# Optimization experiments

Measured on AMD Instinct MI355X. Metric: run time of the kernel, lower is better.

Reference implementation:

```python
import jax, jax.numpy as jnp
import numpy as np

E = 1024        # embedding_dim
H = 16          # num_heads
DR = 1          # downsample_rate
INT = E // DR   # internal_dim
HD = INT // H   # head dim
B, NQ, NK = 4, 2048, 2048


def setup_inputs() -> dict:
    key = jax.random.key(0)
    ks = jax.random.split(key, 11)
    s_in = 1.0 / np.sqrt(E)
    s_int = 1.0 / np.sqrt(INT)
    return {
        "q": jax.random.normal(ks[0], (B, NQ, E), jnp.float32),
        "k": jax.random.normal(ks[1], (B, NK, E), jnp.float32),
        "v": jax.random.normal(ks[2], (B, NK, E), jnp.float32),
        "wq": jax.random.normal(ks[3], (E, INT), jnp.float32) * s_in,
        "bq": jnp.zeros((INT,), jnp.float32),
        "wk": jax.random.normal(ks[4], (E, INT), jnp.float32) * s_in,
        "bk": jnp.zeros((INT,), jnp.float32),
        "wv": jax.random.normal(ks[5], (E, INT), jnp.float32) * s_in,
        "bv": jnp.zeros((INT,), jnp.float32),
        "wo": jax.random.normal(ks[6], (INT, E), jnp.float32) * s_int,
        "bo": jnp.zeros((E,), jnp.float32),
    }


def _heads(x):
    # (B, N, INT) -> (B, H, N, HD)
    b, n, c = x.shape
    return x.reshape(b, n, H, c // H).transpose(0, 2, 1, 3)


def reference(q, k, v, wq, bq, wk, bk, wv, bv, wo, bo):
    qh = _heads(q @ wq + bq)          # (B,H,NQ,HD)
    kh = _heads(k @ wk + bk)          # (B,H,NK,HD)
    vh = _heads(v @ wv + bv)          # (B,H,NK,HD)
    scale = 1.0 / np.sqrt(HD)
    attn = jnp.einsum('bhqd,bhkd->bhqk', qh, kh) * scale  # (B,H,NQ,NK)
    attn = jax.nn.softmax(attn, axis=-1)
    out = jnp.einsum('bhqk,bhkd->bhqd', attn, vh)          # (B,H,NQ,HD)
    out = out.transpose(0, 2, 1, 3).reshape(q.shape[0], qh.shape[2], INT)
    return out @ wo + bo
```

## Files before the change

kernel.cpp:

```cpp
#include <hip/hip_runtime.h>
#include <hip/hip_bf16.h>
#include <cstdint>
#include <cstddef>

typedef __bf16 bf16_t;
typedef __bf16 bf16x8 __attribute__((ext_vector_type(8)));
typedef float f32x4 __attribute__((ext_vector_type(4)));
typedef float f32x16 __attribute__((ext_vector_type(16)));
typedef uint32_t u32;

#define EDIM 1024
#define HH 16
#define HD 64
#define NSEQ 2048
#define QSCALE 0.18033688011f

__device__ __forceinline__ void async_copy16(const bf16_t* gsrc, bf16_t* lds_dst) {
    __builtin_amdgcn_global_load_lds(
        (const __attribute__((address_space(1))) uint32_t*)gsrc,
        (__attribute__((address_space(3))) uint32_t*)lds_dst,
        16, 0, 0);
}

__device__ __forceinline__ bf16x8 cvt8(float4 x, float4 y) {
    bf16x8 v = {(bf16_t)x.x, (bf16_t)x.y, (bf16_t)x.z, (bf16_t)x.w,
                (bf16_t)y.x, (bf16_t)y.y, (bf16_t)y.z, (bf16_t)y.w};
    return v;
}

__global__ void cvt3_f32_bf16(const float* __restrict__ q, const float* __restrict__ k,
                              const float* __restrict__ v,
                              bf16_t* __restrict__ xq, bf16_t* __restrict__ xk,
                              bf16_t* __restrict__ xv) {
    const float* in;
    bf16_t* out;
    switch (blockIdx.y) {
        case 0: in = q; out = xq; break;
        case 1: in = k; out = xk; break;
        default: in = v; out = xv; break;
    }
    size_t i = ((size_t)blockIdx.x * 256 + threadIdx.x) * 8;
    float4 x = *(const float4*)(in + i);
    float4 y = *(const float4*)(in + i + 4);
    *(bf16x8*)(out + i) = cvt8(x, y);
}

__global__ void transpose_all(const float* __restrict__ w0, const float* __restrict__ w1,
                              const float* __restrict__ w2, const float* __restrict__ w3,
                              bf16_t* __restrict__ o0, bf16_t* __restrict__ o1,
                              bf16_t* __restrict__ o2, bf16_t* __restrict__ o3) {
    __shared__ bf16_t t[64][65];
    const float* in;
    bf16_t* out;
    switch (blockIdx.z) {
        case 0: in = w0; out = o0; break;
        case 1: in = w1; out = o1; break;
        case 2: in = w2; out = o2; break;
        default: in = w3; out = o3; break;
    }
    const int tid = threadIdx.x;
    const int kt = blockIdx.x, nt = blockIdx.y;
    #pragma unroll
    for (int i = 0; i < 16; i++) {
        int idx = i * 256 + tid;
        int r = idx >> 6, c = idx & 63;
        t[r][c] = (bf16_t)in[(size_t)(kt * 64 + r) * 1024 + nt * 64 + c];
    }
    __syncthreads();
    #pragma unroll
    for (int i = 0; i < 16; i++) {
        int idx = i * 256 + tid;
        int r = idx >> 6, c = idx & 63;
        out[(size_t)(nt * 64 + r) * 1024 + kt * 64 + c] = t[c][r];
    }
}

__global__ __launch_bounds__(256, 2)
void gemm_qkv_async(const bf16_t* __restrict__ Xq, const bf16_t* __restrict__ Xk,
                    const bf16_t* __restrict__ Xv,
                    const bf16_t* __restrict__ Wq, const bf16_t* __restrict__ Wk,
                    const bf16_t* __restrict__ Wv,
                    const float* __restrict__ bq, const float* __restrict__ bk,
                    const float* __restrict__ bv,
                    bf16_t* __restrict__ Qh, bf16_t* __restrict__ Kh,
                    bf16_t* __restrict__ Vt) {
    constexpr int BM = 128, BN = 128, BK = 64, K = 1024, NT = K / BK;
    __shared__ bf16_t Asm[2][BM * BK];
    __shared__ bf16_t Bsm[2][BN * BK];
    const int tid = threadIdx.x;
    const int wave = tid >> 6, lane = tid & 63;
    const int quad = lane >> 4, l15 = lane & 15;
    const int bx = blockIdx.x, by = blockIdx.y;
    const int mt = (by >> 3) * 8 + bx;
    const int n0 = (by & 7) * BN;
    const int wt = mt >> 6;
    const int m0 = (mt - wt * 64) * BM;
    const int wm = (wave & 1) * 64, wn = (wave >> 1) * 64;

    const bf16_t* A    = wt == 0 ? Xq : (wt == 1 ? Xk : Xv);
    const bf16_t* Bt   = wt == 0 ? Wq : (wt == 1 ? Wk : Wv);
    const float*  bias = wt == 0 ? bq : (wt == 1 ? bk : bv);
    bf16_t*       Cout = wt == 0 ? Qh : (wt == 1 ? Kh : Vt);
    const float oscale = wt == 0 ? QSCALE : 1.0f;

    f32x4 acc[4][4] = {};

    auto stage = [&](int t, int buf) {
        const int k0 = t * BK;
        #pragma unroll
        for (int i = 0; i < 4; i++) {
            int s = i * 256 + tid;
            int row = s >> 3, kc = (s & 7) ^ (row & 7);
            async_copy16(A + (size_t)(m0 + row) * K + k0 + kc * 8, &Asm[buf][s * 8]);
        }
        #pragma unroll
        for (int i = 0; i < 4; i++) {
            int s = i * 256 + tid;
            int row = s >> 3, kc = (s & 7) ^ (row & 7);
            async_copy16(Bt + (size_t)(n0 + row) * K + k0 + kc * 8, &Bsm[buf][s * 8]);
        }
    };

    stage(0, 0);
    stage(1, 1);
    asm volatile("s_waitcnt vmcnt(8)" ::: "memory");
    __builtin_amdgcn_s_barrier();
    __builtin_amdgcn_sched_barrier(0);

    for (int t = 0; t < NT; ++t) {
        const int buf = t & 1;
        bf16x8 af[2][4], bfr[2][4];
        #pragma unroll
        for (int ks = 0; ks < 2; ks++) {
            #pragma unroll
            for (int mi = 0; mi < 4; mi++) {
                int row = wm + mi * 16 + l15;
                int g = ks * 4 + quad;
                af[ks][mi] = *(const bf16x8*)&Asm[buf][row * BK + ((g ^ (row & 7)) * 8)];
            }
            #pragma unroll
            for (int ni = 0; ni < 4; ni++) {
                int row = wn + ni * 16 + l15;
                int g = ks * 4 + quad;
                bfr[ks][ni] = *(const bf16x8*)&Bsm[buf][row * BK + ((g ^ (row & 7)) * 8)];
            }
        }
        #pragma unroll
        for (int ks = 0; ks < 2; ks++)
            #pragma unroll
            for (int mi = 0; mi < 4; mi++)
                #pragma unroll
                for (int ni = 0; ni < 4; ni++)
                    acc[mi][ni] = __builtin_amdgcn_mfma_f32_16x16x32_bf16(
                        af[ks][mi], bfr[ks][ni], acc[mi][ni], 0, 0, 0);

        if (t + 1 < NT) {
            __builtin_amdgcn_s_barrier();
            __builtin_amdgcn_sched_barrier(0);
            if (t + 2 < NT) {
                stage(t + 2, buf);
                asm volatile("s_waitcnt vmcnt(8)" ::: "memory");
            } else {
                asm volatile("s_waitcnt vmcnt(0)" ::: "memory");
            }
            asm volatile("s_waitcnt lgkmcnt(0)" ::: "memory");
            __builtin_amdgcn_s_barrier();
            __builtin_amdgcn_sched_barrier(0);
        }
    }

    #pragma unroll
    for (int mi = 0; mi < 4; mi++) {
        #pragma unroll
        for (int ni = 0; ni < 4; ni++) {
            #pragma unroll
            for (int r = 0; r < 4; r++) {
                int m = m0 + wm + mi * 16 + quad * 4 + r;
                int nch = n0 + wn + ni * 16 + l15;
                float v = (acc[mi][ni][r] + bias[nch]) * oscale;
                int b = m >> 11, n = m & 2047;
                int h = nch >> 6, d = nch & 63;
                if (wt < 2)
                    Cout[(((size_t)(b * HH + h)) * NSEQ + n) * HD + d] = (bf16_t)v;
                else
                    Cout[(((size_t)(b * HH + h)) * HD + d) * NSEQ + n] = (bf16_t)v;
            }
        }
    }
}

__global__ __launch_bounds__(256, 2)
void gemm_qkv(const float* __restrict__ Aq, const float* __restrict__ Ak,
              const float* __restrict__ Av,
              const bf16_t* __restrict__ Wq, const bf16_t* __restrict__ Wk,
              const bf16_t* __restrict__ Wv,
              const float* __restrict__ bq, const float* __restrict__ bk,
              const float* __restrict__ bv,
              bf16_t* __restrict__ Qh, bf16_t* __restrict__ Kh,
              bf16_t* __restrict__ Vt) {
    constexpr int BM = 128, BN = 128, BK = 64, K = 1024, NT = K / BK;
    __shared__ bf16_t Asm[2][BM * BK];
    __shared__ bf16_t Bsm[2][BN * BK];
    const int tid = threadIdx.x;
    const int wave = tid >> 6, lane = tid & 63;
    const int quad = lane >> 4, l15 = lane & 15;
    const int bx = blockIdx.x, by = blockIdx.y;
    const int mt = (by >> 3) * 8 + bx;
    const int n0 = (by & 7) * BN;
    const int wt = mt >> 6;
    const int m0 = (mt - wt * 64) * BM;
    const int wm = (wave & 1) * 64, wn = (wave >> 1) * 64;

    const float*  A    = wt == 0 ? Aq : (wt == 1 ? Ak : Av);
    const bf16_t* Bt   = wt == 0 ? Wq : (wt == 1 ? Wk : Wv);
    const float*  bias = wt == 0 ? bq : (wt == 1 ? bk : bv);
    bf16_t*       Cout = wt == 0 ? Qh : (wt == 1 ? Kh : Vt);
    const float oscale = wt == 0 ? QSCALE : 1.0f;

    f32x4 acc[4][4] = {};
    float4 ar[8];

    auto loadA = [&](int t) {
        const int k0 = t * BK;
        #pragma unroll
        for (int i = 0; i < 4; i++) {
            int s = i * 256 + tid;
            int row = s >> 3, kc = (s & 7) ^ (row & 7);
            const float* sp = A + (size_t)(m0 + row) * K + k0 + kc * 8;
            ar[2 * i]     = *(const float4*)sp;
            ar[2 * i + 1] = *(const float4*)(sp + 4);
        }
    };
    auto writeA = [&](int buf) {
        #pragma unroll
        for (int i = 0; i < 4; i++) {
            int s = i * 256 + tid;
            *(bf16x8*)&Asm[buf][s * 8] = cvt8(ar[2 * i], ar[2 * i + 1]);
        }
    };
    auto stageB = [&](int t, int buf) {
        const int k0 = t * BK;
        #pragma unroll
        for (int i = 0; i < 4; i++) {
            int s = i * 256 + tid;
            int row = s >> 3, kc = (s & 7) ^ (row & 7);
            async_copy16(Bt + (size_t)(n0 + row) * K + k0 + kc * 8, &Bsm[buf][s * 8]);
        }
    };

    loadA(0);
    stageB(0, 0);
    writeA(0);
    stageB(1, 1);
    asm volatile("s_waitcnt vmcnt(4)" ::: "memory");
    loadA(1);
    asm volatile("s_waitcnt lgkmcnt(0)" ::: "memory");
    __builtin_amdgcn_s_barrier();
    __builtin_amdgcn_sched_barrier(0);

    for (int t = 0; t < NT; ++t) {
        const int buf = t & 1;
        bf16x8 af[2][4], bfr[2][4];
        #pragma unroll
        for (int ks = 0; ks < 2; ks++) {
            #pragma unroll
            for (int mi = 0; mi < 4; mi++) {
                int row = wm + mi * 16 + l15;
                int g = ks * 4 + quad;
                af[ks][mi] = *(const bf16x8*)&Asm[buf][row * BK + ((g ^ (row & 7)) * 8)];
            }
            #pragma unroll
            for (int ni = 0; ni < 4; ni++) {
                int row = wn + ni * 16 + l15;
                int g = ks * 4 + quad;
                bfr[ks][ni] = *(const bf16x8*)&Bsm[buf][row * BK + ((g ^ (row & 7)) * 8)];
            }
        }
        #pragma unroll
        for (int ks = 0; ks < 2; ks++)
            #pragma unroll
            for (int mi = 0; mi < 4; mi++)
                #pragma unroll
                for (int ni = 0; ni < 4; ni++)
                    acc[mi][ni] = __builtin_amdgcn_mfma_f32_16x16x32_bf16(
                        af[ks][mi], bfr[ks][ni], acc[mi][ni], 0, 0, 0);

        if (t + 1 < NT) {
            __builtin_amdgcn_s_barrier();
            __builtin_amdgcn_sched_barrier(0);
            writeA(buf ^ 1);
            if (t + 2 < NT) {
                stageB(t + 2, buf);
                asm volatile("s_waitcnt vmcnt(4)" ::: "memory");
                loadA(t + 2);
            } else {
                asm volatile("s_waitcnt vmcnt(0)" ::: "memory");
            }
            asm volatile("s_waitcnt lgkmcnt(0)" ::: "memory");
            __builtin_amdgcn_s_barrier();
            __builtin_amdgcn_sched_barrier(0);
        }
    }

    #pragma unroll
    for (int mi = 0; mi < 4; mi++) {
        #pragma unroll
        for (int ni = 0; ni < 4; ni++) {
            #pragma unroll
            for (int r = 0; r < 4; r++) {
                int m = m0 + wm + mi * 16 + quad * 4 + r;
                int nch = n0 + wn + ni * 16 + l15;
                float v = (acc[mi][ni][r] + bias[nch]) * oscale;
                int b = m >> 11, n = m & 2047;
                int h = nch >> 6, d = nch & 63;
                if (wt < 2)
                    Cout[(((size_t)(b * HH + h)) * NSEQ + n) * HD + d] = (bf16_t)v;
                else
                    Cout[(((size_t)(b * HH + h)) * HD + d) * NSEQ + n] = (bf16_t)v;
            }
        }
    }
}

__global__ __launch_bounds__(256, 2)
void gemm_out(const bf16_t* __restrict__ A, const bf16_t* __restrict__ Bt,
              const float* __restrict__ bias, float* __restrict__ C) {
    constexpr int BM = 128, BN = 128, BK = 64, K = 1024, N = 1024, NT = K / BK;
    __shared__ bf16_t Asm[2][BM * BK];
    __shared__ bf16_t Bsm[2][BN * BK];
    const int tid = threadIdx.x;
    const int wave = tid >> 6, lane = tid & 63;
    const int quad = lane >> 4, l15 = lane & 15;
    const int bx = blockIdx.x, by = blockIdx.y;
    const int n0 = (by & 7) * BN;
    const int m0 = ((by >> 3) * 8 + bx) * BM;
    const int wm = (wave & 1) * 64, wn = (wave >> 1) * 64;

    f32x4 acc[4][4] = {};

    auto stage = [&](int t, int buf) {
        const int k0 = t * BK;
        #pragma unroll
        for (int i = 0; i < 4; i++) {
            int s = i * 256 + tid;
            int row = s >> 3, kc = (s & 7) ^ (row & 7);
            async_copy16(A + (size_t)(m0 + row) * K + k0 + kc * 8, &Asm[buf][s * 8]);
        }
        #pragma unroll
        for (int i = 0; i < 4; i++) {
            int s = i * 256 + tid;
            int row = s >> 3, kc = (s & 7) ^ (row & 7);
            async_copy16(Bt + (size_t)(n0 + row) * K + k0 + kc * 8, &Bsm[buf][s * 8]);
        }
    };

    stage(0, 0);
    stage(1, 1);
    asm volatile("s_waitcnt vmcnt(8)" ::: "memory");
    __builtin_amdgcn_s_barrier();
    __builtin_amdgcn_sched_barrier(0);

    for (int t = 0; t < NT; ++t) {
        const int buf = t & 1;
        bf16x8 af[2][4], bfr[2][4];
        #pragma unroll
        for (int ks = 0; ks < 2; ks++) {
            #pragma unroll
            for (int mi = 0; mi < 4; mi++) {
                int row = wm + mi * 16 + l15;
                int g = ks * 4 + quad;
                af[ks][mi] = *(const bf16x8*)&Asm[buf][row * BK + ((g ^ (row & 7)) * 8)];
            }
            #pragma unroll
            for (int ni = 0; ni < 4; ni++) {
                int row = wn + ni * 16 + l15;
                int g = ks * 4 + quad;
                bfr[ks][ni] = *(const bf16x8*)&Bsm[buf][row * BK + ((g ^ (row & 7)) * 8)];
            }
        }
        #pragma unroll
        for (int ks = 0; ks < 2; ks++)
            #pragma unroll
            for (int mi = 0; mi < 4; mi++)
                #pragma unroll
                for (int ni = 0; ni < 4; ni++)
                    acc[mi][ni] = __builtin_amdgcn_mfma_f32_16x16x32_bf16(
                        af[ks][mi], bfr[ks][ni], acc[mi][ni], 0, 0, 0);

        if (t + 1 < NT) {
            __builtin_amdgcn_s_barrier();
            __builtin_amdgcn_sched_barrier(0);
            if (t + 2 < NT) {
                stage(t + 2, buf);
                asm volatile("s_waitcnt vmcnt(8)" ::: "memory");
            } else {
                asm volatile("s_waitcnt vmcnt(0)" ::: "memory");
            }
            asm volatile("s_waitcnt lgkmcnt(0)" ::: "memory");
            __builtin_amdgcn_s_barrier();
            __builtin_amdgcn_sched_barrier(0);
        }
    }

    #pragma unroll
    for (int mi = 0; mi < 4; mi++) {
        #pragma unroll
        for (int ni = 0; ni < 4; ni++) {
            #pragma unroll
            for (int r = 0; r < 4; r++) {
                int m = m0 + wm + mi * 16 + quad * 4 + r;
                int nch = n0 + wn + ni * 16 + l15;
                C[(size_t)m * N + nch] = acc[mi][ni][r] + bias[nch];
            }
        }
    }
}

union PW { u32 w[4]; bf16x8 v; };

__device__ __forceinline__ u32 pack_bf16(float lo, float hi) {
    union { bf16_t h[2]; u32 u; } x;
    x.h[0] = (bf16_t)lo;
    x.h[1] = (bf16_t)hi;
    return x.u;
}

__device__ __forceinline__ void half_swap(u32& a, u32& b) {
    auto r = __builtin_amdgcn_permlane32_swap(a, b, false, false);
    a = r[0];
    b = r[1];
}

__device__ __forceinline__ void softmax_pack(const f32x16 sa, float* lp,
                                             PW& f0, PW& f1) {
    float p[16];
    #pragma unroll
    for (int r = 0; r < 16; r++) {
        p[r] = __builtin_amdgcn_exp2f(sa[r]);
        lp[r & 3] += p[r];
    }
    u32 x0 = pack_bf16(p[0],  p[1]),  x1 = pack_bf16(p[2],  p[3]);
    u32 x2 = pack_bf16(p[4],  p[5]),  x3 = pack_bf16(p[6],  p[7]);
    u32 x4 = pack_bf16(p[8],  p[9]),  x5 = pack_bf16(p[10], p[11]);
    u32 x6 = pack_bf16(p[12], p[13]), x7 = pack_bf16(p[14], p[15]);
    half_swap(x0, x2); half_swap(x1, x3);
    half_swap(x4, x6); half_swap(x5, x7);
    f0.w[0] = x0; f0.w[1] = x1; f0.w[2] = x2; f0.w[3] = x3;
    f1.w[0] = x4; f1.w[1] = x5; f1.w[2] = x6; f1.w[3] = x7;
}

__global__ __launch_bounds__(256, 4)
void attn_kernel(const bf16_t* __restrict__ Qh, const bf16_t* __restrict__ Kh,
                 const bf16_t* __restrict__ Vt, bf16_t* __restrict__ out) {
    __shared__ bf16_t Ks[2][64 * 64];
    __shared__ bf16_t Vs[2][64 * 64];
    const int tid = threadIdx.x, wave = tid >> 6, lane = tid & 63;
    const int l31 = lane & 31, hi = lane >> 5;
    const int B = blockIdx.x;
    const int qt = (B >> 3) & 15;
    const int bh = (B >> 7) * 8 + (B & 7);
    const int b = bh >> 4, h = bh & 15;

    const bf16_t* kbase = Kh + (size_t)bh * NSEQ * HD;
    const bf16_t* vbase = Vt + (size_t)bh * HD * NSEQ;

    bf16x8 qf[4];
    {
        const bf16_t* qrow =
            Qh + ((size_t)bh * NSEQ + qt * 128 + wave * 32 + l31) * HD + hi * 8;
        #pragma unroll
        for (int s = 0; s < 4; s++) qf[s] = *(const bf16x8*)(qrow + s * 16);
    }

    const bf16_t *ks0, *ks1, *vs0, *vs1;
    {
        int r0 = tid >> 3, c0 = tid & 7;
        int s1 = tid + 256;
        int r1 = s1 >> 3, c1 = s1 & 7;
        ks0 = kbase + r0 * HD + (c0 ^ (r0 & 7)) * 8;
        ks1 = kbase + r1 * HD + (c1 ^ (r1 & 7)) * 8;
        vs0 = vbase + (size_t)r0 * NSEQ + (c0 ^ (r0 & 7)) * 8;
        vs1 = vbase + (size_t)r1 * NSEQ + (c1 ^ (r1 & 7)) * 8;
    }

    async_copy16(ks0, &Ks[0][tid * 8]);
    async_copy16(ks1, &Ks[0][(tid + 256) * 8]);
    async_copy16(vs0, &Vs[0][tid * 8]);
    async_copy16(vs1, &Vs[0][(tid + 256) * 8]);

    f32x16 oacc[2] = {};
    float lp[4] = {};

    for (int t = 0; t < 32; t++) {
        const int cur = t & 1;
        __syncthreads();

        if (t < 31) {
            ks0 += 64 * HD; ks1 += 64 * HD;
            vs0 += 64;      vs1 += 64;
            async_copy16(ks0, &Ks[cur ^ 1][tid * 8]);
            async_copy16(ks1, &Ks[cur ^ 1][(tid + 256) * 8]);
            async_copy16(vs0, &Vs[cur ^ 1][tid * 8]);
            async_copy16(vs1, &Vs[cur ^ 1][(tid + 256) * 8]);
        }

        const f32x16 zero = {};
        f32x16 sacc0, sacc1;
        {
            int g = hi;
            int row0 = l31, row1 = 32 + l31;
            bf16x8 ak0 = *(const bf16x8*)&Ks[cur][row0 * 64 + ((g ^ (row0 & 7)) * 8)];
            bf16x8 ak1 = *(const bf16x8*)&Ks[cur][row1 * 64 + ((g ^ (row1 & 7)) * 8)];
            __builtin_amdgcn_s_setprio(1);
            sacc0 = __builtin_amdgcn_mfma_f32_32x32x16_bf16(ak0, qf[0], zero, 0, 0, 0);
            sacc1 = __builtin_amdgcn_mfma_f32_32x32x16_bf16(ak1, qf[0], zero, 0, 0, 0);
            __builtin_amdgcn_s_setprio(0);
        }
        #pragma unroll
        for (int s = 1; s < 4; s++) {
            int g = s * 2 + hi;
            int row0 = l31;
            int row1 = 32 + l31;
            bf16x8 ak0 = *(const bf16x8*)&Ks[cur][row0 * 64 + ((g ^ (row0 & 7)) * 8)];
            bf16x8 ak1 = *(const bf16x8*)&Ks[cur][row1 * 64 + ((g ^ (row1 & 7)) * 8)];
            __builtin_amdgcn_s_setprio(1);
            sacc0 = __builtin_amdgcn_mfma_f32_32x32x16_bf16(ak0, qf[s], sacc0, 0, 0, 0);
            sacc1 = __builtin_amdgcn_mfma_f32_32x32x16_bf16(ak1, qf[s], sacc1, 0, 0, 0);
            __builtin_amdgcn_s_setprio(0);
        }

        PW pa[4];
        softmax_pack(sacc0, lp, pa[0], pa[1]);
        softmax_pack(sacc1, lp, pa[2], pa[3]);

        #pragma unroll
        for (int dt = 0; dt < 2; dt++) {
            #pragma unroll
            for (int ks = 0; ks < 4; ks++) {
                int row = dt * 32 + l31;
                int g = ks * 2 + hi;
                bf16x8 bv = *(const bf16x8*)&Vs[cur][row * 64 + ((g ^ (row & 7)) * 8)];
                __builtin_amdgcn_s_setprio(1);
                oacc[dt] = __builtin_amdgcn_mfma_f32_32x32x16_bf16(
                    pa[ks].v, bv, oacc[dt], 0, 0, 0);
                __builtin_amdgcn_s_setprio(0);
            }
        }
    }

    float lsum = (lp[0] + lp[1]) + (lp[2] + lp[3]);
    lsum += __shfl_xor(lsum, 32, 64);
    float linv = 1.f / lsum;
    float rinv[16];
    #pragma unroll
    for (int r = 0; r < 16; r++) {
        int q = (r & 3) + 8 * (r >> 2) + 4 * hi;
        rinv[r] = __shfl(linv, q, 64);
    }

    const int n0 = qt * 128 + wave * 32;
    #pragma unroll
    for (int dt = 0; dt < 2; dt++) {
        int c = h * 64 + dt * 32 + l31;
        #pragma unroll
        for (int r = 0; r < 16; r++) {
            int q = (r & 3) + 8 * (r >> 2) + 4 * hi;
            out[((size_t)b * NSEQ + n0 + q) * EDIM + c] = (bf16_t)(oacc[dt][r] * rinv[r]);
        }
    }
}

extern "C" void kernel_launch(void* const* d_in, const int* in_sizes, int n_in,
                              void* d_out, int out_size, void* d_ws, size_t ws_size,
                              hipStream_t stream) {
    const float* q  = (const float*)d_in[0];
    const float* k  = (const float*)d_in[1];
    const float* v  = (const float*)d_in[2];
    const float* wq = (const float*)d_in[3];
    const float* bq = (const float*)d_in[4];
    const float* wk = (const float*)d_in[5];
    const float* bk = (const float*)d_in[6];
    const float* wv = (const float*)d_in[7];
    const float* bv = (const float*)d_in[8];
    const float* wo = (const float*)d_in[9];
    const float* bo = (const float*)d_in[10];
    float* out = (float*)d_out;

    char* ws = (char*)d_ws;
    bf16_t* wqt = (bf16_t*)(ws + ((size_t)0  << 20));
    bf16_t* wkt = (bf16_t*)(ws + ((size_t)2  << 20));
    bf16_t* wvt = (bf16_t*)(ws + ((size_t)4  << 20));
    bf16_t* wot = (bf16_t*)(ws + ((size_t)6  << 20));

    bf16_t* Qh  = (bf16_t*)(ws + ((size_t)8  << 20));
    bf16_t* Kh  = (bf16_t*)(ws + ((size_t)24 << 20));
    bf16_t* Vt  = (bf16_t*)(ws + ((size_t)40 << 20));
    bf16_t* ao  = (bf16_t*)(ws + ((size_t)56 << 20));
    bf16_t* Xq  = (bf16_t*)(ws + ((size_t)72 << 20));
    bf16_t* Xk  = (bf16_t*)(ws + ((size_t)88 << 20));
    bf16_t* Xv  = (bf16_t*)(ws + ((size_t)104 << 20));

    const bool big = ws_size >= ((size_t)120 << 20);

    transpose_all<<<dim3(16, 16, 4), dim3(256), 0, stream>>>(wq, wk, wv, wo,
                                                             wqt, wkt, wvt, wot);

    if (big) {
        cvt3_f32_bf16<<<dim3(4096, 3), dim3(256), 0, stream>>>(q, k, v, Xq, Xk, Xv);
        gemm_qkv_async<<<dim3(8, 192), dim3(256), 0, stream>>>(Xq, Xk, Xv,
                                                               wqt, wkt, wvt,
                                                               bq, bk, bv, Qh, Kh, Vt);
    } else {
        gemm_qkv<<<dim3(8, 192), dim3(256), 0, stream>>>(q, k, v, wqt, wkt, wvt,
                                                         bq, bk, bv, Qh, Kh, Vt);
    }

    attn_kernel<<<1024, dim3(256), 0, stream>>>(Qh, Kh, Vt, ao);

    gemm_out<<<dim3(8, 64), dim3(256), 0, stream>>>(ao, wot, bo, out);
}
```

Measured before the change: 334.4 us.

## Merge prep kernels and compute softmax row sums with an MFMA against ones

Merges the weight-transpose and activation-conversion kernels into a single launch, removing one kernel launch and its tail. In attention, the per-lane scalar accumulation of exp values is replaced by an extra MFMA of the probabilities against a ones vector. That gives row sums already laid out like the output accumulator, so the final cross-lane shuffles are dropped. Launch bounds for the attention kernel are relaxed from 4 to 2 waves per SIMD, giving it more registers for the extra accumulator at the possible cost of occupancy.

Result: slower. 344.6 us (+3.1%).

```diff
diff --git a/kernel.cpp b/kernel.cpp
--- a/kernel.cpp
+++ b/kernel.cpp
@@ -28,50 +28,56 @@
     return v;
 }
 
-__global__ void cvt3_f32_bf16(const float* __restrict__ q, const float* __restrict__ k,
-                              const float* __restrict__ v,
-                              bf16_t* __restrict__ xq, bf16_t* __restrict__ xk,
-                              bf16_t* __restrict__ xv) {
-    const float* in;
-    bf16_t* out;
-    switch (blockIdx.y) {
-        case 0: in = q; out = xq; break;
-        case 1: in = k; out = xk; break;
-        default: in = v; out = xv; break;
-    }
-    size_t i = ((size_t)blockIdx.x * 256 + threadIdx.x) * 8;
-    float4 x = *(const float4*)(in + i);
-    float4 y = *(const float4*)(in + i + 4);
-    *(bf16x8*)(out + i) = cvt8(x, y);
-}
-
-__global__ void transpose_all(const float* __restrict__ w0, const float* __restrict__ w1,
-                              const float* __restrict__ w2, const float* __restrict__ w3,
-                              bf16_t* __restrict__ o0, bf16_t* __restrict__ o1,
-                              bf16_t* __restrict__ o2, bf16_t* __restrict__ o3) {
+__global__ void prep(const float* __restrict__ w0, const float* __restrict__ w1,
+                     const float* __restrict__ w2, const float* __restrict__ w3,
+                     bf16_t* __restrict__ o0, bf16_t* __restrict__ o1,
+                     bf16_t* __restrict__ o2, bf16_t* __restrict__ o3,
+                     const float* __restrict__ q, const float* __restrict__ k,
+                     const float* __restrict__ v,
+                     bf16_t* __restrict__ xq, bf16_t* __restrict__ xk,
+                     bf16_t* __restrict__ xv, int do_cvt) {
     __shared__ bf16_t t[64][65];
-    const float* in;
-    bf16_t* out;
-    switch (blockIdx.z) {
-        case 0: in = w0; out = o0; break;
-        case 1: in = w1; out = o1; break;
-        case 2: in = w2; out = o2; break;
-        default: in = w3; out = o3; break;
-    }
+    const int id = blockIdx.x;
     const int tid = threadIdx.x;
-    const int kt = blockIdx.x, nt = blockIdx.y;
-    #pragma unroll
-    for (int i = 0; i < 16; i++) {
-        int idx = i * 256 + tid;
-        int r = idx >> 6, c = idx & 63;
-        t[r][c] = (bf16_t)in[(size_t)(kt * 64 + r) * 1024 + nt * 64 + c];
-    }
-    __syncthreads();
-    #pragma unroll
-    for (int i = 0; i < 16; i++) {
-        int idx = i * 256 + tid;
-        int r = idx >> 6, c = idx & 63;
-        out[(size_t)(nt * 64 + r) * 1024 + kt * 64 + c] = t[c][r];
+    if (id < 1024) {
+        const int z = id >> 8, rem = id & 255, kt = rem >> 4, nt = rem & 15;
+        const float* in;
+        bf16_t* out;
+        switch (z) {
+            case 0: in = w0; out = o0; break;
+            case 1: in = w1; out = o1; break;
+            case 2: in = w2; out = o2; break;
+            default: in = w3; out = o3; break;
+        }
+        #pragma unroll
+        for (int i = 0; i < 16; i++) {
+            int idx = i * 256 + tid;
+            int r = idx >> 6, c = idx & 63;
+            t[r][c] = (bf16_t)in[(size_t)(kt * 64 + r) * 1024 + nt * 64 + c];
+        }
+        __syncthreads();
+        #pragma unroll
+        for (int i = 0; i < 16; i++) {
+            int idx = i * 256 + tid;
+            int r = idx >> 6, c = idx & 63;
+            out[(size_t)(nt * 64 + r) * 1024 + kt * 64 + c] = t[c][r];
+        }
+    } else {
+        if (!do_cvt) return;
+        const int j = id - 1024;
+        const int which = j >> 12;
+        const int blk = j & 4095;
+        const float* in;
+        bf16_t* out;
+        switch (which) {
+            case 0: in = q; out = xq; break;
+            case 1: in = k; out = xk; break;
+            default: in = v; out = xv; break;
+        }
+        size_t i = ((size_t)blk * 256 + tid) * 8;
+        float4 x = *(const float4*)(in + i);
+        float4 y = *(const float4*)(in + i + 4);
+        *(bf16x8*)(out + i) = cvt8(x, y);
     }
 }
 
@@ -431,14 +437,11 @@
     b = r[1];
 }
 
-__device__ __forceinline__ void softmax_pack(const f32x16 sa, float* lp,
-                                             PW& f0, PW& f1) {
+__device__ __forceinline__ void softmax_pack(const f32x16 sa, PW& f0, PW& f1) {
     float p[16];
     #pragma unroll
-    for (int r = 0; r < 16; r++) {
+    for (int r = 0; r < 16; r++)
         p[r] = __builtin_amdgcn_exp2f(sa[r]);
-        lp[r & 3] += p[r];
-    }
     u32 x0 = pack_bf16(p[0],  p[1]),  x1 = pack_bf16(p[2],  p[3]);
     u32 x2 = pack_bf16(p[4],  p[5]),  x3 = pack_bf16(p[6],  p[7]);
     u32 x4 = pack_bf16(p[8],  p[9]),  x5 = pack_bf16(p[10], p[11]);
@@ -449,7 +452,7 @@
     f1.w[0] = x4; f1.w[1] = x5; f1.w[2] = x6; f1.w[3] = x7;
 }
 
-__global__ __launch_bounds__(256, 4)
+__global__ __launch_bounds__(256, 2)
 void attn_kernel(const bf16_t* __restrict__ Qh, const bf16_t* __restrict__ Kh,
                  const bf16_t* __restrict__ Vt, bf16_t* __restrict__ out) {
     __shared__ bf16_t Ks[2][64 * 64];
@@ -488,8 +491,12 @@
     async_copy16(vs0, &Vs[0][tid * 8]);
     async_copy16(vs1, &Vs[0][(tid + 256) * 8]);
 
+    bf16x8 onesv;
+    #pragma unroll
+    for (int j = 0; j < 8; j++) onesv[j] = (bf16_t)1.0f;
+
     f32x16 oacc[2] = {};
-    float lp[4] = {};
+    f32x16 oacc_l = {};
 
     for (int t = 0; t < 32; t++) {
         const int cur = t & 1;
@@ -530,8 +537,15 @@
         }
 
         PW pa[4];
-        softmax_pack(sacc0, lp, pa[0], pa[1]);
-        softmax_pack(sacc1, lp, pa[2], pa[3]);
+        softmax_pack(sacc0, pa[0], pa[1]);
+        softmax_pack(sacc1, pa[2], pa[3]);
+
+        __builtin_amdgcn_s_setprio(1);
+        #pragma unroll
+        for (int ks = 0; ks < 4; ks++)
+            oacc_l = __builtin_amdgcn_mfma_f32_32x32x16_bf16(
+                pa[ks].v, onesv, oacc_l, 0, 0, 0);
+        __builtin_amdgcn_s_setprio(0);
 
         #pragma unroll
         for (int dt = 0; dt < 2; dt++) {
@@ -548,15 +562,9 @@
         }
     }
 
-    float lsum = (lp[0] + lp[1]) + (lp[2] + lp[3]);
-    lsum += __shfl_xor(lsum, 32, 64);
-    float linv = 1.f / lsum;
     float rinv[16];
     #pragma unroll
-    for (int r = 0; r < 16; r++) {
-        int q = (r & 3) + 8 * (r >> 2) + 4 * hi;
-        rinv[r] = __shfl(linv, q, 64);
-    }
+    for (int r = 0; r < 16; r++) rinv[r] = 1.f / oacc_l[r];
 
     const int n0 = qt * 128 + wave * 32;
     #pragma unroll
@@ -602,11 +610,10 @@
 
     const bool big = ws_size >= ((size_t)120 << 20);
 
-    transpose_all<<<dim3(16, 16, 4), dim3(256), 0, stream>>>(wq, wk, wv, wo,
-                                                             wqt, wkt, wvt, wot);
+    prep<<<dim3(13312), dim3(256), 0, stream>>>(wq, wk, wv, wo, wqt, wkt, wvt, wot,
+                                                q, k, v, Xq, Xk, Xv, big ? 1 : 0);
 
     if (big) {
-        cvt3_f32_bf16<<<dim3(4096, 3), dim3(256), 0, stream>>>(q, k, v, Xq, Xk, Xv);
         gemm_qkv_async<<<dim3(8, 192), dim3(256), 0, stream>>>(Xq, Xk, Xv,
                                                                wqt, wkt, wvt,
                                                                bq, bk, bv, Qh, Kh, Vt);
```
